# Kernel optimization log

Hardware: AMD Instinct MI355X
Metric: run time of the kernel (lower is better)

Reference implementation:

```python
import jax, jax.numpy as jnp
import numpy as np
from jax import lax

B, S, C, H, T = 64, 256, 64, 512, 128  # batch, enc seq, coord_dims, hidden, target_len

def _lstm_step(Wih, Whh, b, h, c, xt):
    # PyTorch gate order: i, f, g, o
    g = xt @ Wih.T + h @ Whh.T + b
    i, f, gg, o = jnp.split(g, 4, axis=-1)
    i = jax.nn.sigmoid(i); f = jax.nn.sigmoid(f)
    gg = jnp.tanh(gg); o = jax.nn.sigmoid(o)
    c = f * c + i * gg
    h = o * jnp.tanh(c)
    return h, c

def _lstm_layer(x_seq, Wih, Whh, b):
    # x_seq: [B, S, D] -> outputs [B, S, H], final (h, c)
    Bsz = x_seq.shape[0]
    h0 = jnp.zeros((Bsz, Whh.shape[1]), x_seq.dtype)
    c0 = jnp.zeros_like(h0)
    def step(carry, xt):
        h, c = carry
        h, c = _lstm_step(Wih, Whh, b, h, c, xt)
        return (h, c), h
    (hT, cT), ys = lax.scan(step, (h0, c0), x_seq.swapaxes(0, 1))
    return ys.swapaxes(0, 1), hT, cT

def setup_inputs() -> dict:
    key = jax.random.key(0)
    ks = jax.random.split(key, 16)
    s = 1.0 / np.sqrt(H)
    def u(k, shape):
        return jax.random.uniform(k, shape, jnp.float32, -s, s)
    inp = {"x": jax.random.normal(ks[0], (B, S, C), jnp.float32), "target_len": T}
    inp["enc_Wih0"] = u(ks[1], (4 * H, C)); inp["enc_Whh0"] = u(ks[2], (4 * H, H)); inp["enc_b0"] = u(ks[3], (4 * H,))
    inp["enc_Wih1"] = u(ks[4], (4 * H, H)); inp["enc_Whh1"] = u(ks[5], (4 * H, H)); inp["enc_b1"] = u(ks[6], (4 * H,))
    inp["dec_Wih0"] = u(ks[7], (4 * H, C)); inp["dec_Whh0"] = u(ks[8], (4 * H, H)); inp["dec_b0"] = u(ks[9], (4 * H,))
    inp["dec_Wih1"] = u(ks[10], (4 * H, H)); inp["dec_Whh1"] = u(ks[11], (4 * H, H)); inp["dec_b1"] = u(ks[12], (4 * H,))
    inp["lin_W"] = u(ks[13], (C, H)); inp["lin_b"] = u(ks[14], (C,))
    return inp

def reference(x, enc_Wih0, enc_Whh0, enc_b0, enc_Wih1, enc_Whh1, enc_b1,
              dec_Wih0, dec_Whh0, dec_b0, dec_Wih1, dec_Whh1, dec_b1,
              lin_W, lin_b, target_len):
    # ---- encoder: 2-layer LSTM over full sequence ----
    y0, h0, c0 = _lstm_layer(x, enc_Wih0, enc_Whh0, enc_b0)
    _, h1, c1 = _lstm_layer(y0, enc_Wih1, enc_Whh1, enc_b1)
    dec_in0 = x[:, -1, :]  # [B, C]
    def step(carry, _):
        xin, h0_, c0_, h1_, c1_ = carry
        h0n, c0n = _lstm_step(dec_Wih0, dec_Whh0, dec_b0, h0_, c0_, xin)
        h1n, c1n = _lstm_step(dec_Wih1, dec_Whh1, dec_b1, h1_, c1_, h0n)
        out = h1n @ lin_W.T + lin_b  # [B, C]
        return (out, h0n, c0n, h1n, c1n), out
    _, outs = lax.scan(step, (dec_in0, h0, c0, h1, c1), None, length=target_len)
    return outs.swapaxes(0, 1)  # [B, target_len, C]
```

## Files before the change

### kernel.cpp

```cpp
#include <hip/hip_runtime.h>

typedef _Float16 f16;
typedef _Float16 f16x4 __attribute__((ext_vector_type(4)));
typedef _Float16 f16x8 __attribute__((ext_vector_type(8)));
typedef float    f32x4 __attribute__((ext_vector_type(4)));

#define MFMA16(a,b,c) __builtin_amdgcn_mfma_f32_16x16x32_f16((a),(b),(c),0,0,0)

constexpr unsigned NB = 64, NS = 256, NC = 64, NH = 512, NT = 128;
constexpr unsigned HSLOT = NB * NH;

constexpr unsigned OFF_WX   = 0;
constexpr unsigned OFF_WLIN = OFF_WX   + NB*NS*NC*2;
constexpr unsigned OFF_EH0  = OFF_WLIN + NC*NH*2;
constexpr unsigned OFF_EH1  = OFF_EH0  + 2*HSLOT*2;
constexpr unsigned OFF_DH0  = OFF_EH1  + 2*HSLOT*2;
constexpr unsigned OFF_DH1  = OFF_DH0  + 2*HSLOT*2;
constexpr unsigned OFF_BAR  = OFF_DH1  + 2*HSLOT*2;


__global__ void prep_convert(const float* __restrict__ x,
                             const float* __restrict__ linw,
                             char* __restrict__ ws)
{
    unsigned rel = blockIdx.x * 256u + threadIdx.x;
    if (rel < 65536u) {
        unsigned t = rel >> 8, c4 = (rel >> 4) & 15u, b0 = (rel & 15u) << 2;
        #pragma unroll
        for (unsigned j = 0; j < 4; ++j) {
            float4 v = ((const float4*)x)[(b0 + j) * 4096u + t * 16u + c4];
            f16x4 o; o[0]=(f16)v.x; o[1]=(f16)v.y; o[2]=(f16)v.z; o[3]=(f16)v.w;
            ((f16x4*)(ws + OFF_WX))[t * 1024u + c4 * 64u + b0 + j] = o;
        }
    } else if ((rel -= 65536u) < 8192u) {
        float4 v = ((const float4*)linw)[rel];
        f16x4 o; o[0]=(f16)v.x; o[1]=(f16)v.y; o[2]=(f16)v.z; o[3]=(f16)v.w;
        ((f16x4*)(ws + OFF_WLIN))[rel] = o;
    } else if ((rel -= 8192u) < 32768u) {
        f16x8 z = {};
        ((f16x8*)(ws + OFF_EH0))[rel] = z;
    } else if ((rel -= 32768u) < 512u) {
        int4 z; z.x = z.y = z.z = z.w = 0;
        ((int4*)(ws + OFF_BAR))[rel] = z;
    }
}


__device__ __forceinline__ float sigm(float v)   { return 1.f / (1.f + __expf(-v)); }
__device__ __forceinline__ float tanh_f(float v) { return 2.f / (1.f + __expf(-2.f * v)) - 1.f; }

__device__ __forceinline__ void h_store8(f16* p, f16x4 v)
{
    union { unsigned long long u; f16x4 h; } c; c.h = v;
    __hip_atomic_store((unsigned long long*)p, c.u, __ATOMIC_RELAXED, __HIP_MEMORY_SCOPE_AGENT);
}
__device__ __forceinline__ f16x4 h_load8(const f16* p)
{
    unsigned long long v = __hip_atomic_load((const unsigned long long*)p,
                                             __ATOMIC_RELAXED, __HIP_MEMORY_SCOPE_AGENT);
    union { unsigned long long u; f16x4 h; } c; c.u = v;
    return c.h;
}
__device__ __forceinline__ f16x8 h_load_blk(const f16* slot, int kr, int m)
{
    const f16* p = slot + ((kr >> 2) << 8) + (m << 2);
    f16x4 a = h_load8(p);
    f16x4 b = h_load8(p + 256);
    f16x8 r;
    r[0]=a[0]; r[1]=a[1]; r[2]=a[2]; r[3]=a[3];
    r[4]=b[0]; r[5]=b[1]; r[6]=b[2]; r[7]=b[3];
    return r;
}

__device__ __forceinline__ void grid_barrier(int* bar, int wg, int tid, int& bgen)
{
    __syncthreads();
    if (tid == 0) {
        const int dom = wg & 3;
        const int idx = ((wg >> 7) << 5) | ((wg >> 2) & 31);
        const int sub = idx >> 4;
        int* cnt  = bar + (dom * 4 + sub) * 32;
        int* flg  = bar + 512 + (dom * 4) * 32;
        const int gen = bgen + 1;

        int old = __hip_atomic_fetch_add(cnt, 1, __ATOMIC_RELAXED, __HIP_MEMORY_SCOPE_AGENT);
        if (old == (gen << 4) - 1)
            __hip_atomic_store(flg + sub * 32, gen, __ATOMIC_RELAXED, __HIP_MEMORY_SCOPE_AGENT);
        for (;;) {
            int a = __hip_atomic_load(flg +  0, __ATOMIC_RELAXED, __HIP_MEMORY_SCOPE_AGENT);
            int b = __hip_atomic_load(flg + 32, __ATOMIC_RELAXED, __HIP_MEMORY_SCOPE_AGENT);
            int c = __hip_atomic_load(flg + 64, __ATOMIC_RELAXED, __HIP_MEMORY_SCOPE_AGENT);
            int d = __hip_atomic_load(flg + 96, __ATOMIC_RELAXED, __HIP_MEMORY_SCOPE_AGENT);
            if (a >= gen && b >= gen && c >= gen && d >= gen) break;
            __builtin_amdgcn_s_sleep(1);
        }
        bgen = gen;
    }
    __syncthreads();
}

__device__ __forceinline__ void load_wlds_f32(f16 (*Wlds)[1032],
                                              const float* __restrict__ A, int KA,
                                              const float* __restrict__ Bs, int KB,
                                              int u0, int tid)
{
    int nch = (KA + KB) >> 2;
    int tot = nch << 6;
    for (int idx = tid; idx < tot; idx += 256) {
        int j = idx / nch, ch = idx - j * nch;
        int k = ch << 2;
        int grow = ((j >> 4) << 9) + u0 + (j & 15);
        float4 v;
        if (k < KA) v = *(const float4*)(A + grow * KA + k);
        else        v = *(const float4*)(Bs + grow * KB + (k - KA));
        f16x4 o; o[0]=(f16)v.x; o[1]=(f16)v.y; o[2]=(f16)v.z; o[3]=(f16)v.w;
        *(f16x4*)&Wlds[j][k] = o;
    }
}

__device__ __forceinline__ void load_wlds_fold(f16 (*Wlds)[1032],
                                               const float* __restrict__ dwih0,
                                               const float* __restrict__ linw,
                                               const float* __restrict__ dwhh0,
                                               int u0, int tid)
{
    #pragma unroll
    for (int rep = 0; rep < 4; ++rep) {
        int idx = ((rep << 8) + tid) << 5;
        int j = idx >> 9, k0 = idx & 511;
        int grow = ((j >> 4) << 9) + u0 + (j & 15);
        float acc[32];
        #pragma unroll
        for (int q = 0; q < 32; ++q) acc[q] = 0.f;
        for (int c = 0; c < 64; ++c) {
            float wc = dwih0[grow * 64 + c];
            const float* lr = linw + c * 512 + k0;
            #pragma unroll
            for (int q = 0; q < 32; ++q) acc[q] += wc * lr[q];
        }
        #pragma unroll
        for (int q = 0; q < 32; ++q) Wlds[j][k0 + q] = (f16)acc[q];
    }
    int tot = 8192;
    for (int idx = tid; idx < tot; idx += 256) {
        int j = idx >> 7, ch = idx & 127, k = ch << 2;
        int grow = ((j >> 4) << 9) + u0 + (j & 15);
        float4 v = *(const float4*)(dwhh0 + grow * 512 + k);
        f16x4 o; o[0]=(f16)v.x; o[1]=(f16)v.y; o[2]=(f16)v.z; o[3]=(f16)v.w;
        *(f16x4*)&Wlds[j][512 + k] = o;
    }
}

__device__ __forceinline__ void gemm_acc4(f16 (*Wlds)[1032],
                                          const f16* __restrict__ A0, int kOff,
                                          f32x4& ac0, f32x4& ac1, f32x4& ac2, f32x4& ac3,
                                          int b0, int tid)
{
    const int lane = tid & 63, wv = tid >> 6, q = lane >> 4, lo = lane & 15;
    const int s0 = wv << 2;
    f16x8 A[4];
    #pragma unroll
    for (int s = 0; s < 4; ++s) {
        int kr = ((s0 + s) << 5) + (q << 3);
        A[s] = h_load_blk(A0, kr, b0 + lo);
    }
    __builtin_amdgcn_sched_barrier(0);
    #pragma unroll
    for (int s = 0; s < 4; ++s) {
        int kk = kOff + ((s0 + s) << 5) + (q << 3);
        ac0 = MFMA16(A[s], *(const f16x8*)&Wlds[lo     ][kk], ac0);
        ac1 = MFMA16(A[s], *(const f16x8*)&Wlds[lo + 16][kk], ac1);
        ac2 = MFMA16(A[s], *(const f16x8*)&Wlds[lo + 32][kk], ac2);
        ac3 = MFMA16(A[s], *(const f16x8*)&Wlds[lo + 48][kk], ac3);
    }
}

__device__ __forceinline__ void finish_round(float (*Dp)[16][68],
                                             f32x4 ac0, f32x4 ac1, f32x4 ac2, f32x4 ac3,
                                             const float* ba, float& creg,
                                             f16* __restrict__ ho,
                                             int u0, int b0, int tid)
{
    const int lane = tid & 63, wv = tid >> 6, q = lane >> 4, lo = lane & 15;
    #pragma unroll
    for (int r = 0; r < 4; ++r) {
        int rr = (q << 2) + r;
        Dp[wv][rr][lo     ] = ac0[r];
        Dp[wv][rr][lo + 16] = ac1[r];
        Dp[wv][rr][lo + 32] = ac2[r];
        Dp[wv][rr][lo + 48] = ac3[r];
    }
    __syncthreads();
    const int b = tid >> 4, u = tid & 15;
    float v[4];
    #pragma unroll
    for (int g = 0; g < 4; ++g) {
        int col = (g << 4) + u;
        v[g] = Dp[0][b][col] + Dp[1][b][col] + Dp[2][b][col] + Dp[3][b][col] + ba[g];
    }
    float ii = sigm(v[0]), ff = sigm(v[1]), gg = tanh_f(v[2]), oo = sigm(v[3]);
    creg = ff * creg + ii * gg;
    float h = oo * tanh_f(creg);
    float h1 = __shfl_down(h, 1);
    float h2 = __shfl_down(h, 2);
    float h3 = __shfl_down(h, 3);
    if ((u & 3) == 0) {
        f16x4 hv; hv[0] = (f16)h; hv[1] = (f16)h1; hv[2] = (f16)h2; hv[3] = (f16)h3;
        h_store8(ho + (((u0 + u) >> 2) << 8) + ((b0 + b) << 2), hv);
    }
}

template<int MAXS, bool EXACT>
__device__ __forceinline__ void rnn_round(f16 (*Wlds)[1032], float (*Dp)[16][68],
                                          const f16* __restrict__ A0, int K0,
                                          const f16* __restrict__ A1,
                                          int K, int kStart,
                                          const float* ba, float& creg,
                                          f16* __restrict__ ho,
                                          int u0, int b0, int tid)
{
    const int lane = tid & 63, wv = tid >> 6, q = lane >> 4, lo = lane & 15;
    const int sBeg = kStart >> 5, n = (K >> 5) - sBeg;
    const int per = n >> 2, rem = n & 3;
    const int s0 = sBeg + wv * per + (wv < rem ? wv : rem);
    const int ns = EXACT ? MAXS : (per + (wv < rem ? 1 : 0));

    int sEff[MAXS];
    #pragma unroll
    for (int s = 0; s < MAXS; ++s)
        sEff[s] = s0 + (EXACT ? s : (s < ns ? s : ns - 1));

    f16x8 A[MAXS];
    #pragma unroll
    for (int s = 0; s < MAXS; ++s) {
        int kb = sEff[s] << 5;
        bool in0 = kb < K0;
        const f16* src = in0 ? A0 : A1;
        int kr = (in0 ? kb : kb - K0) + (q << 3);
        A[s] = h_load_blk(src, kr, b0 + lo);
    }
    if (!EXACT) {
        if (MAXS - 1 >= ns) { f16x8 z = {}; A[MAXS-1] = z; }
    }
    __builtin_amdgcn_sched_barrier(0);

    f32x4 ac0 = {0.f,0.f,0.f,0.f}, ac1 = ac0, ac2 = ac0, ac3 = ac0;
    #pragma unroll
    for (int s = 0; s < MAXS; ++s) {
        int kk = (sEff[s] << 5) + (q << 3);
        ac0 = MFMA16(A[s], *(const f16x8*)&Wlds[lo     ][kk], ac0);
        ac1 = MFMA16(A[s], *(const f16x8*)&Wlds[lo + 16][kk], ac1);
        ac2 = MFMA16(A[s], *(const f16x8*)&Wlds[lo + 32][kk], ac2);
        ac3 = MFMA16(A[s], *(const f16x8*)&Wlds[lo + 48][kk], ac3);
    }
    finish_round(Dp, ac0, ac1, ac2, ac3, ba, creg, ho, u0, b0, tid);
}

__device__ __forceinline__ void out_gemm(const f16* __restrict__ H1,
                                         const f16* __restrict__ LW,
                                         const float* __restrict__ linb,
                                         float* __restrict__ out,
                                         int w, int t, int tid)
{
    const int lane = tid & 63, wv = tid >> 6, q = lane >> 4, lo = lane & 15;
    int b0 = w << 4;
    f32x4 ac = {0.f,0.f,0.f,0.f};
    int c0 = wv << 4;

    f16x8 a[16];
    #pragma unroll
    for (int s = 0; s < 16; ++s)
        a[s] = h_load_blk(H1, (s << 5) + (q << 3), b0 + lo);
    __builtin_amdgcn_sched_barrier(0);

    #pragma unroll
    for (int s = 0; s < 16; ++s) {
        int kk = (s << 5) + (q << 3);
        f16x8 bf = *(const f16x8*)(LW + (c0 + lo) * 512 + kk);
        ac = MFMA16(a[s], bf, ac);
    }
    float lb = linb[c0 + lo];
    #pragma unroll
    for (int r = 0; r < 4; ++r) {
        int b = b0 + (q << 2) + r;
        out[(size_t)b * (NT * NC) + t * NC + c0 + lo] = ac[r] + lb;
    }
}


__global__ void __launch_bounds__(256)
lstm_main(char* __restrict__ ws,
          const float* __restrict__ x,
          const float* __restrict__ wih0, const float* __restrict__ whh0, const float* __restrict__ eb0,
          const float* __restrict__ wih1, const float* __restrict__ whh1, const float* __restrict__ eb1,
          const float* __restrict__ dwih0, const float* __restrict__ dwhh0, const float* __restrict__ db0,
          const float* __restrict__ dwih1, const float* __restrict__ dwhh1, const float* __restrict__ db1,
          const float* __restrict__ linw, const float* __restrict__ linb,
          float* __restrict__ out)
{
    __shared__ f16   Wlds[64][1032];
    __shared__ float Dp[4][16][68];

    const int wg = blockIdx.x, tid = threadIdx.x;
    const bool isL0 = wg < 128;
    const int wl = wg & 127;
    const int b0 = (wl & 3) << 4;
    const int u0 = (wl >> 2) << 4;
    const int u  = tid & 15;
    int* bar = (int*)(ws + OFF_BAR);
    int bgen = 0;

    const f16* WX   = (const f16*)(ws + OFF_WX);
    const f16* WLIN = (const f16*)(ws + OFF_WLIN);
    f16* EH0 = (f16*)(ws + OFF_EH0);
    f16* EH1 = (f16*)(ws + OFF_EH1);
    f16* DH0 = (f16*)(ws + OFF_DH0);
    f16* DH1 = (f16*)(ws + OFF_DH1);

    if (isL0) load_wlds_f32(Wlds, wih0,  64, whh0, 512, u0, tid);
    else      load_wlds_f32(Wlds, wih1, 512, whh1, 512, u0, tid);
    __syncthreads();

    float ba[4];
    {
        const float* bs = isL0 ? eb0 : eb1;
        #pragma unroll
        for (int g = 0; g < 4; ++g) ba[g] = bs[(g << 9) + u0 + u];
    }
    float creg = 0.f;

    for (int r = 0; r <= (int)NS; ++r) {
        if (isL0 && r < (int)NS) {
            rnn_round<5,false>(Wlds, Dp,
                      WX + r * 4096, 64,
                      EH0 + ((r + 1) & 1) * HSLOT,
                      576, 0, ba, creg,
                      EH0 + (r & 1) * HSLOT, u0, b0, tid);
        } else if (!isL0 && r >= 1) {
            int t = r - 1;
            rnn_round<8,true>(Wlds, Dp,
                      EH0 + (t & 1) * HSLOT, 512,
                      EH1 + ((t + 1) & 1) * HSLOT,
                      1024, 0, ba, creg,
                      EH1 + (t & 1) * HSLOT, u0, b0, tid);
        }
        grid_barrier(bar, wg, tid, bgen);
    }

    float baI[4];
    if (isL0) {
        load_wlds_fold(Wlds, dwih0, linw, dwhh0, u0, tid);
        const int bb = b0 + (tid >> 4);
        const float* xr = x + bb * (NS * NC) + (NS - 1) * NC;
        #pragma unroll
        for (int g = 0; g < 4; ++g) {
            int row = (g << 9) + u0 + u;
            const float* wr = dwih0 + row * 64;
            float bsum = 0.f, xsum = 0.f;
            for (int c = 0; c < 64; ++c) { bsum += linb[c] * wr[c]; xsum += xr[c] * wr[c]; }
            ba[g]  = db0[row] + bsum;
            baI[g] = db0[row] + xsum;
        }
    } else {
        load_wlds_f32(Wlds, dwih1, 512, dwhh1, 512, u0, tid);
        #pragma unroll
        for (int g = 0; g < 4; ++g) { ba[g] = db1[(g << 9) + u0 + u]; baI[g] = 0.f; }
    }
    __syncthreads();

    f32x4 c0 = {0.f,0.f,0.f,0.f}, c1 = c0, c2 = c0, c3 = c0;
    const f32x4 zero = {0.f,0.f,0.f,0.f};

    for (int d = 0; d < 2 * (int)NT; ++d) {
        int t = d >> 1;
        if ((d & 1) == 0) {
            if (isL0) {
                if (t == 0) {
                    f32x4 a0 = zero, a1 = zero, a2 = zero, a3 = zero;
                    gemm_acc4(Wlds, EH0 + HSLOT, 512, a0, a1, a2, a3, b0, tid);
                    finish_round(Dp, a0, a1, a2, a3, baI, creg, DH0, u0, b0, tid);
                } else {
                    f32x4 a0 = c0, a1 = c1, a2 = c2, a3 = c3;
                    gemm_acc4(Wlds, DH1 + ((t + 1) & 1) * HSLOT, 0, a0, a1, a2, a3, b0, tid);
                    finish_round(Dp, a0, a1, a2, a3, ba, creg,
                                 DH0 + (t & 1) * HSLOT, u0, b0, tid);
                }
            } else {
                const f16* h1p = (t == 0) ? EH1 + HSLOT : DH1 + ((t + 1) & 1) * HSLOT;
                c0 = zero; c1 = zero; c2 = zero; c3 = zero;
                gemm_acc4(Wlds, h1p, 512, c0, c1, c2, c3, b0, tid);
                if (wg < 132 && t >= 1)
                    out_gemm(DH1 + ((t - 1) & 1) * HSLOT, WLIN, linb, out, wg - 128, t - 1, tid);
            }
        } else {
            if (!isL0) {
                f32x4 a0 = c0, a1 = c1, a2 = c2, a3 = c3;
                gemm_acc4(Wlds, DH0 + (t & 1) * HSLOT, 0, a0, a1, a2, a3, b0, tid);
                finish_round(Dp, a0, a1, a2, a3, ba, creg,
                             DH1 + (t & 1) * HSLOT, u0, b0, tid);
            } else if (t < (int)NT - 1) {
                c0 = zero; c1 = zero; c2 = zero; c3 = zero;
                gemm_acc4(Wlds, DH0 + (t & 1) * HSLOT, 512, c0, c1, c2, c3, b0, tid);
            }
        }
        grid_barrier(bar, wg, tid, bgen);
    }

    if (!isL0 && wg < 132)
        out_gemm(DH1 + HSLOT, WLIN, linb, out, wg - 128, (int)NT - 1, tid);
}


extern "C" void kernel_launch(void* const* d_in, const int* in_sizes, int n_in,
                              void* d_out, int out_size, void* d_ws, size_t ws_size,
                              hipStream_t stream)
{
    const float* x     = (const float*)d_in[0];
    const float* wih0  = (const float*)d_in[2];
    const float* whh0  = (const float*)d_in[3];
    const float* eb0   = (const float*)d_in[4];
    const float* wih1  = (const float*)d_in[5];
    const float* whh1  = (const float*)d_in[6];
    const float* eb1   = (const float*)d_in[7];
    const float* dwih0 = (const float*)d_in[8];
    const float* dwhh0 = (const float*)d_in[9];
    const float* db0   = (const float*)d_in[10];
    const float* dwih1 = (const float*)d_in[11];
    const float* dwhh1 = (const float*)d_in[12];
    const float* db1   = (const float*)d_in[13];
    const float* linw  = (const float*)d_in[14];
    const float* linb  = (const float*)d_in[15];
    char* ws    = (char*)d_ws;
    float* outp = (float*)d_out;

    prep_convert<<<418, 256, 0, stream>>>(x, linw, ws);

    lstm_main<<<256, 256, 0, stream>>>(ws, x, wih0, whh0, eb0, wih1, whh1, eb1,
                                       dwih0, dwhh0, db0, dwih1, dwhh1, db1,
                                       linw, linb, outp);
}
```

Before: 1.923 ms.

## Make decoder barriers producer-only and pack barrier flags into 64-bit loads

Replaces the all-workgroup grid barrier with a round sync in which, during decoder phases, only the workgroups that produce the hidden state for that phase increment counters. Everyone still waits on the flags. The four per-domain flags are packed contiguously so one poll takes two 64-bit loads instead of four strided 32-bit loads. The aim is to cut atomic traffic and arrival latency on the serial critical path. The risk is correctness, since it relies on the consumer-only groups not writing anything that later readers depend on before the flag advances.

```diff
diff --git a/kernel.cpp b/kernel.cpp
--- a/kernel.cpp
+++ b/kernel.cpp
@@ -72,29 +72,30 @@
     return r;
 }
 
-__device__ __forceinline__ void grid_barrier(int* bar, int wg, int tid, int& bgen)
+__device__ __forceinline__ void sync_round(int* bar, int dom, bool producer,
+                                           int sub, int addPerSub,
+                                           int tid, int& gen, int& cbase)
 {
     __syncthreads();
     if (tid == 0) {
-        const int dom = wg & 3;
-        const int idx = ((wg >> 7) << 5) | ((wg >> 2) & 31);
-        const int sub = idx >> 4;
-        int* cnt  = bar + (dom * 4 + sub) * 32;
-        int* flg  = bar + 512 + (dom * 4) * 32;
-        const int gen = bgen + 1;
-
-        int old = __hip_atomic_fetch_add(cnt, 1, __ATOMIC_RELAXED, __HIP_MEMORY_SCOPE_AGENT);
-        if (old == (gen << 4) - 1)
-            __hip_atomic_store(flg + sub * 32, gen, __ATOMIC_RELAXED, __HIP_MEMORY_SCOPE_AGENT);
+        gen   += 1;
+        cbase += addPerSub;
+        int* flg = bar + 1024 + dom * 32;
+        if (producer) {
+            int* cnt = bar + (dom * 4 + sub) * 32;
+            int old = __hip_atomic_fetch_add(cnt, 1, __ATOMIC_RELAXED, __HIP_MEMORY_SCOPE_AGENT);
+            if (old == cbase - 1)
+                __hip_atomic_store(flg + sub, gen, __ATOMIC_RELAXED, __HIP_MEMORY_SCOPE_AGENT);
+        }
+        const unsigned long long* flg64 = (const unsigned long long*)flg;
         for (;;) {
-            int a = __hip_atomic_load(flg +  0, __ATOMIC_RELAXED, __HIP_MEMORY_SCOPE_AGENT);
-            int b = __hip_atomic_load(flg + 32, __ATOMIC_RELAXED, __HIP_MEMORY_SCOPE_AGENT);
-            int c = __hip_atomic_load(flg + 64, __ATOMIC_RELAXED, __HIP_MEMORY_SCOPE_AGENT);
-            int d = __hip_atomic_load(flg + 96, __ATOMIC_RELAXED, __HIP_MEMORY_SCOPE_AGENT);
+            unsigned long long v0 = __hip_atomic_load(flg64 + 0, __ATOMIC_RELAXED, __HIP_MEMORY_SCOPE_AGENT);
+            unsigned long long v1 = __hip_atomic_load(flg64 + 1, __ATOMIC_RELAXED, __HIP_MEMORY_SCOPE_AGENT);
+            int a = (int)v0, b = (int)(v0 >> 32);
+            int c = (int)v1, d = (int)(v1 >> 32);
             if (a >= gen && b >= gen && c >= gen && d >= gen) break;
             __builtin_amdgcn_s_sleep(1);
         }
-        bgen = gen;
     }
     __syncthreads();
 }
@@ -306,9 +307,13 @@
     const int wl = wg & 127;
     const int b0 = (wl & 3) << 4;
     const int u0 = (wl >> 2) << 4;
+    const int ug = wl >> 2;
+    const int dom = wl & 3;
     const int u  = tid & 15;
+    const int encSub = (((wg >> 7) << 5) | ug) >> 4;
+    const int decSub = ug >> 3;
     int* bar = (int*)(ws + OFF_BAR);
-    int bgen = 0;
+    int gen = 0, cbase = 0;
 
     const f16* WX   = (const f16*)(ws + OFF_WX);
     const f16* WLIN = (const f16*)(ws + OFF_WLIN);
@@ -344,7 +349,7 @@
                       1024, 0, ba, creg,
                       EH1 + (t & 1) * HSLOT, u0, b0, tid);
         }
-        grid_barrier(bar, wg, tid, bgen);
+        sync_round(bar, dom, true, encSub, 16, tid, gen, cbase);
     }
 
     float baI[4];
@@ -392,6 +397,7 @@
                 if (wg < 132 && t >= 1)
                     out_gemm(DH1 + ((t - 1) & 1) * HSLOT, WLIN, linb, out, wg - 128, t - 1, tid);
             }
+            sync_round(bar, dom, isL0, decSub, 8, tid, gen, cbase);
         } else {
             if (!isL0) {
                 f32x4 a0 = c0, a1 = c1, a2 = c2, a3 = c3;
@@ -402,8 +408,8 @@
                 c0 = zero; c1 = zero; c2 = zero; c3 = zero;
                 gemm_acc4(Wlds, DH0 + (t & 1) * HSLOT, 512, c0, c1, c2, c3, b0, tid);
             }
-        }
-        grid_barrier(bar, wg, tid, bgen);
+            sync_round(bar, dom, !isL0, decSub, 8, tid, gen, cbase);
+        }
     }
 
     if (!isL0 && wg < 132)
```

New measurement: 1.872 ms. 2.6% less time.

## Replace grid-wide counter barrier with per-domain producer flag synchronization

Applied to the files above, without the earlier changes.

The grid barrier, which used an atomic counter plus four sub-flags, is replaced with per-workgroup generation flags grouped by batch domain. In each round, producers store their own flag and 64 lanes poll all the flags they depend on in parallel. In the decoder phases, only the layer that produced data signals and only the consumers wait on it. This removes atomic fetch-add contention and the extra hop through the counter, and narrows synchronization to the workgroups that share a batch slice. The risk is ordering and buffer-reuse hazards, since the ordering that every workgroup used to wait for is now implicit.

```diff
diff --git a/kernel.cpp b/kernel.cpp
--- a/kernel.cpp
+++ b/kernel.cpp
@@ -72,29 +72,18 @@
     return r;
 }
 
-__device__ __forceinline__ void grid_barrier(int* bar, int wg, int tid, int& bgen)
+__device__ __forceinline__ void sync_flags(int* flg, bool producer, int mySlot,
+                                           int pollBase, int pollMask,
+                                           int tid, int& gen)
 {
     __syncthreads();
-    if (tid == 0) {
-        const int dom = wg & 3;
-        const int idx = ((wg >> 7) << 5) | ((wg >> 2) & 31);
-        const int sub = idx >> 4;
-        int* cnt  = bar + (dom * 4 + sub) * 32;
-        int* flg  = bar + 512 + (dom * 4) * 32;
-        const int gen = bgen + 1;
-
-        int old = __hip_atomic_fetch_add(cnt, 1, __ATOMIC_RELAXED, __HIP_MEMORY_SCOPE_AGENT);
-        if (old == (gen << 4) - 1)
-            __hip_atomic_store(flg + sub * 32, gen, __ATOMIC_RELAXED, __HIP_MEMORY_SCOPE_AGENT);
-        for (;;) {
-            int a = __hip_atomic_load(flg +  0, __ATOMIC_RELAXED, __HIP_MEMORY_SCOPE_AGENT);
-            int b = __hip_atomic_load(flg + 32, __ATOMIC_RELAXED, __HIP_MEMORY_SCOPE_AGENT);
-            int c = __hip_atomic_load(flg + 64, __ATOMIC_RELAXED, __HIP_MEMORY_SCOPE_AGENT);
-            int d = __hip_atomic_load(flg + 96, __ATOMIC_RELAXED, __HIP_MEMORY_SCOPE_AGENT);
-            if (a >= gen && b >= gen && c >= gen && d >= gen) break;
+    const int g = ++gen;
+    if (tid < 64) {
+        if (producer && tid == 0)
+            __hip_atomic_store(flg + mySlot, g, __ATOMIC_RELAXED, __HIP_MEMORY_SCOPE_AGENT);
+        int* myf = flg + pollBase + (tid & pollMask);
+        while (__hip_atomic_load(myf, __ATOMIC_RELAXED, __HIP_MEMORY_SCOPE_AGENT) < g)
             __builtin_amdgcn_s_sleep(1);
-        }
-        bgen = gen;
     }
     __syncthreads();
 }
@@ -306,9 +295,12 @@
     const int wl = wg & 127;
     const int b0 = (wl & 3) << 4;
     const int u0 = (wl >> 2) << 4;
+    const int ug = wl >> 2;
+    const int dom = wl & 3;
     const int u  = tid & 15;
-    int* bar = (int*)(ws + OFF_BAR);
-    int bgen = 0;
+    const int mySlot = (isL0 ? 0 : 32) + ug;
+    int* flg = (int*)(ws + OFF_BAR) + dom * 64;
+    int gen = 0;
 
     const f16* WX   = (const f16*)(ws + OFF_WX);
     const f16* WLIN = (const f16*)(ws + OFF_WLIN);
@@ -344,7 +336,7 @@
                       1024, 0, ba, creg,
                       EH1 + (t & 1) * HSLOT, u0, b0, tid);
         }
-        grid_barrier(bar, wg, tid, bgen);
+        sync_flags(flg, true, mySlot, 0, 63, tid, gen);
     }
 
     float baI[4];
@@ -392,6 +384,7 @@
                 if (wg < 132 && t >= 1)
                     out_gemm(DH1 + ((t - 1) & 1) * HSLOT, WLIN, linb, out, wg - 128, t - 1, tid);
             }
+            sync_flags(flg, isL0, mySlot, 0, 31, tid, gen);
         } else {
             if (!isL0) {
                 f32x4 a0 = c0, a1 = c1, a2 = c2, a3 = c3;
@@ -402,8 +395,8 @@
                 c0 = zero; c1 = zero; c2 = zero; c3 = zero;
                 gemm_acc4(Wlds, DH0 + (t & 1) * HSLOT, 512, c0, c1, c2, c3, b0, tid);
             }
+            sync_flags(flg, !isL0, mySlot, 32, 31, tid, gen);
         }
-        grid_barrier(bar, wg, tid, bgen);
     }
 
     if (!isL0 && wg < 132)
```

Result: slower. 2.104 ms (+9.4%).
